# Optimization experiments

Measured on AMD Instinct MI355X. Metric: run time of the kernel, lower is better.

Reference implementation:

```python
import jax, jax.numpy as jnp
import numpy as np

PATCH_NUM = 10  # self.patch_num divisor
TOP_N = 5


def _extract_patches(feat, ps):
    """feat: [1,C,H,W] -> [P, C*ps*ps] with P = (H-ps)*(W-ps), matching the
    original loop over h in range(H-ps), w in range(W-ps)."""
    C, H, W = feat.shape[1:]
    Hm, Wm = H - ps, W - ps
    shifts = [feat[0, :, i:i + Hm, j:j + Wm] for i in range(ps) for j in range(ps)]
    patches = jnp.stack(shifts, axis=1)          # [C, ps*ps, Hm, Wm]
    return patches.reshape(C * ps * ps, Hm * Wm).T  # [P, K], P index = h*Wm + w


def _scale_loss(src_f, tgt_f, pos, ps):
    C = src_f.shape[1]
    K = C * ps * ps
    patches = _extract_patches(src_f, ps)  # [P, K]

    def per_target(p):
        th, tw = p[0], p[1]
        tpatch = jax.lax.dynamic_slice(tgt_f, (0, 0, th, tw), (1, C, ps, ps)).reshape(K)
        dist = jnp.sum(jnp.abs(patches - tpatch), axis=1)  # [P] summed L1 per patch
        _, ids = jax.lax.top_k(-dist, TOP_N)                # 5 nearest patches
        sel = patches[ids]                                   # [TOP_N, K]
        # sum over top-n of mean-L1, each divided by top_n (as in original)
        return jnp.sum(jnp.mean(jnp.abs(sel - tpatch), axis=1)) / TOP_N

    # sequential map over the small number of target patches keeps peak memory
    # at one [P,K] abs-diff buffer per step
    return jnp.sum(jax.lax.map(per_target, pos))


def setup_inputs() -> dict:
    key = jax.random.key(0)
    k0, k1, k2, k3, k4, k5 = jax.random.split(key, 6)
    return {
        "src_f0": jax.random.normal(k0, (1, 64, 256, 256), dtype=jnp.float32),
        "tgt_f0": jax.random.normal(k1, (1, 64, 256, 256), dtype=jnp.float32),
        "src_f1": jax.random.normal(k2, (1, 128, 128, 128), dtype=jnp.float32),
        "tgt_f1": jax.random.normal(k3, (1, 128, 128, 128), dtype=jnp.float32),
        "pos0": jax.random.randint(k4, (10, 2), 0, 253, dtype=jnp.int32),
        "pos1": jax.random.randint(k5, (5, 2), 0, 127, dtype=jnp.int32),
    }


def reference(src_f0, tgt_f0, src_f1, tgt_f1, pos0, pos1):
    loss = _scale_loss(src_f0, tgt_f0, pos0, 3) + _scale_loss(src_f1, tgt_f1, pos1, 1)
    return loss / PATCH_NUM
```

## Files before the change

kernel.cpp:

```cpp
#include <hip/hip_runtime.h>
#include <hip/hip_bf16.h>

#define BIG 3.4e38f


__device__ __forceinline__ void merge5(float a[5], const float* b) {
    float r[5];
#pragma unroll
    for (int k = 0; k < 5; ++k) {
        float best = BIG;
#pragma unroll
        for (int i = 0; i <= k + 1; ++i) {
            const int j = k + 1 - i;
            float va = (i == 0) ? -BIG : a[i - 1];
            float vb = (j == 0) ? -BIG : b[j - 1];
            best = fminf(best, fmaxf(va, vb));
        }
        r[k] = best;
    }
#pragma unroll
    for (int k = 0; k < 5; ++k) a[k] = r[k];
}

__device__ __forceinline__ void top5_insert(float m[5], float d) {
    if (d < m[4]) {
        m[4] = d;
#pragma unroll
        for (int k = 4; k > 0; --k) {
            float lo = fminf(m[k - 1], m[k]);
            float hi = fmaxf(m[k - 1], m[k]);
            m[k - 1] = lo;
            m[k] = hi;
        }
    }
}

__device__ __forceinline__ void wave_merge_top5(float m[5]) {
#pragma unroll
    for (int off = 1; off < 64; off <<= 1) {
        float o[5];
#pragma unroll
        for (int k = 0; k < 5; ++k) o[k] = __shfl_xor(m[k], off, 64);
        merge5(m, o);
    }
}

__device__ __forceinline__ bool block_merge_top5(float m[5], float (*s_top)[5],
                                                 float r[5]) {
    const int wid = threadIdx.x >> 6;
    if ((threadIdx.x & 63) == 0) {
#pragma unroll
        for (int k = 0; k < 5; ++k) s_top[wid][k] = m[k];
    }
    __syncthreads();
    if (threadIdx.x == 0) {
#pragma unroll
        for (int k = 0; k < 5; ++k) r[k] = s_top[0][k];
        merge5(r, s_top[1]);
        merge5(r, s_top[2]);
        merge5(r, s_top[3]);
        return true;
    }
    return false;
}

template <int CCH>
__global__ __launch_bounds__(256) void dist0_kernel(
    const float* __restrict__ src, const float* __restrict__ tgt,
    const int* __restrict__ pos, float* __restrict__ dist) {
    constexpr int H = 256, W = 256, HW = H * W, T = 10;
    constexpr int PLANE = 253 * 256;
    const int c0 = blockIdx.y * CCH;
    __shared__ float tl[T * CCH * 3 * 4];

    for (int idx = threadIdx.x; idx < T * CCH * 9; idx += 256) {
        int t = idx / (CCH * 9);
        int rem = idx - t * CCH * 9;
        int cc = rem / 9;
        int r2 = rem - cc * 9;
        int i = r2 / 3, j = r2 - i * 3;
        int th = pos[2 * t], tw = pos[2 * t + 1];
        tl[((t * CCH + cc) * 3 + i) * 4 + j] =
            tgt[(size_t)(c0 + cc) * HW + (th + i) * W + (tw + j)];
    }
    __syncthreads();

    const int tx = threadIdx.x & 63;
    const int ty = threadIdx.x >> 6;
    const int h = blockIdx.x * 4 + ty;
    const int hl = (h <= 250) ? h : 250;
    const int w0 = tx * 4;
    const int bw = (w0 <= 248) ? w0 + 4 : 248;

    float acc[T][4];
#pragma unroll
    for (int t = 0; t < T; ++t)
#pragma unroll
        for (int n = 0; n < 4; ++n) acc[t][n] = 0.f;

    const float* sb = src + (size_t)c0 * HW + hl * W;
    for (int cc = 0; cc < CCH; ++cc) {
        const float* row0 = sb + (size_t)cc * HW;
#pragma unroll
        for (int i = 0; i < 3; ++i) {
            const float4 a = *(const float4*)(row0 + i * W + w0);
            const float2 b = *(const float2*)(row0 + i * W + bw);
            const float r[6] = {a.x, a.y, a.z, a.w, b.x, b.y};
#pragma unroll
            for (int t = 0; t < T; ++t) {
                const float4 tv =
                    *(const float4*)&tl[((t * CCH + cc) * 3 + i) * 4];
#pragma unroll
                for (int n = 0; n < 4; ++n)
                    acc[t][n] += fabsf(r[n] - tv.x) + fabsf(r[n + 1] - tv.y) +
                                 fabsf(r[n + 2] - tv.z);
            }
        }
    }

    if (h < 253) {
        float* dp = dist + (size_t)blockIdx.y * T * PLANE + h * 256 + w0;
#pragma unroll
        for (int t = 0; t < T; ++t) {
            float4 o = {acc[t][0], acc[t][1], acc[t][2], acc[t][3]};
            *(float4*)(dp + (size_t)t * PLANE) = o;
        }
    }
}

template <int CCH>
__global__ __launch_bounds__(256) void dist1_kernel(
    const float* __restrict__ src, const float* __restrict__ tgt,
    const int* __restrict__ pos, float* __restrict__ dist) {
    constexpr int H = 128, W = 128, HW = H * W, T = 5;
    constexpr int PLANE = 127 * 128;
    const int c0 = blockIdx.y * CCH;
    __shared__ float tl[T * CCH];
    for (int idx = threadIdx.x; idx < T * CCH; idx += 256) {
        int t = idx / CCH, cc = idx - t * CCH;
        tl[idx] = tgt[(size_t)(c0 + cc) * HW + pos[2 * t] * W + pos[2 * t + 1]];
    }
    __syncthreads();

    const int w = threadIdx.x & 127;
    const int h = blockIdx.x * 2 + (threadIdx.x >> 7);
    float acc[T] = {0.f, 0.f, 0.f, 0.f, 0.f};
    const float* sp = src + (size_t)c0 * HW + h * W + w;
    for (int cc = 0; cc < CCH; ++cc) {
        const float v = sp[(size_t)cc * HW];
#pragma unroll
        for (int t = 0; t < T; ++t) acc[t] += fabsf(v - tl[t * CCH + cc]);
    }
    if (h < 127) {
        float* dp = dist + (size_t)blockIdx.y * T * PLANE + h * 128 + w;
#pragma unroll
        for (int t = 0; t < T; ++t) dp[(size_t)t * PLANE] = acc[t];
    }
}

template <int PLANE, int ROWW, int VALIDW, int NCH, int T, int NB>
__global__ __launch_bounds__(256) void top5_stage_kernel(
    const float* __restrict__ dist, float* __restrict__ part2) {
    __shared__ float s_top[4][5];
    const int t = blockIdx.y;
    constexpr int NF = PLANE / 4;
    constexpr int ITERS = (NF + NB * 256 - 1) / (NB * 256);
    float m[5] = {BIG, BIG, BIG, BIG, BIG};
#pragma unroll
    for (int k = 0; k < ITERS; ++k) {
        const int f = blockIdx.x * (ITERS * 256) + k * 256 + threadIdx.x;
        if (f < NF) {
            float4 s = *(const float4*)&dist[(size_t)t * PLANE + f * 4];
#pragma unroll
            for (int ch = 1; ch < NCH; ++ch) {
                float4 u =
                    *(const float4*)&dist[((size_t)ch * T + t) * PLANE + f * 4];
                s.x += u.x; s.y += u.y; s.z += u.z; s.w += u.w;
            }
            const int w0 = (f * 4) & (ROWW - 1);
            top5_insert(m, (w0 + 0 < VALIDW) ? s.x : BIG);
            top5_insert(m, (w0 + 1 < VALIDW) ? s.y : BIG);
            top5_insert(m, (w0 + 2 < VALIDW) ? s.z : BIG);
            top5_insert(m, (w0 + 3 < VALIDW) ? s.w : BIG);
        }
    }
    wave_merge_top5(m);
    float r[5];
    if (block_merge_top5(m, s_top, r)) {
        float* dst = part2 + (t * NB + blockIdx.x) * 5;
#pragma unroll
        for (int k = 0; k < 5; ++k) dst[k] = r[k];
    }
}

__global__ __launch_bounds__(256) void final_merge_kernel(
    const float* __restrict__ p2a, int na,
    const float* __restrict__ p2b, int nb,
    unsigned int* __restrict__ out) {
    __shared__ float s_sum[15];
    const int lane = threadIdx.x & 63;
    const int wv = threadIdx.x >> 6;
#pragma unroll
    for (int rt = 0; rt < 4; ++rt) {
        const int t = wv * 4 + rt;
        if (t < 15) {
            const float* base = (t < 10) ? p2a + t * na : p2b + (t - 10) * nb;
            const int n = (t < 10) ? na : nb;
            const float scale =
                (t < 10) ? 1.f / (576.f * 5.f) : 1.f / (128.f * 5.f);
            float m[5] = {BIG, BIG, BIG, BIG, BIG};
            for (int b0 = 0; b0 < n; b0 += 64)
                if (b0 + lane < n) top5_insert(m, base[b0 + lane]);
            wave_merge_top5(m);
            if (lane == 0)
                s_sum[t] = (m[0] + m[1] + m[2] + m[3] + m[4]) * scale;
        }
    }
    __syncthreads();
    if (threadIdx.x == 0) {
        float total = 0.f;
#pragma unroll
        for (int t = 0; t < 15; ++t) total += s_sum[t];
        union { float f; unsigned int i; } uf;
        uf.f = total * 0.1f;
        unsigned int bf = (uf.i + 0x7FFFu + ((uf.i >> 16) & 1u)) >> 16;
        out[0] = (uf.i & 0xFFFF0000u) | (bf & 0xFFFFu);
    }
}

template <int C, int H, int PS, int WM>
__global__ __launch_bounds__(256) void dist_top5_kernel(
    const float* __restrict__ src, const float* __restrict__ tgt,
    const int* __restrict__ pos, float* __restrict__ part) {
    constexpr int W = H;
    constexpr int K = C * PS * PS;
    constexpr int P = WM * WM;
    __shared__ float tlv[K];
    __shared__ float s_top[4][5];
    const int t = blockIdx.y;
    const int th = pos[2 * t], tw = pos[2 * t + 1];
    for (int idx = threadIdx.x; idx < K; idx += 256) {
        int c = idx / (PS * PS);
        int rem = idx - c * PS * PS;
        int i = rem / PS, j = rem - i * PS;
        tlv[idx] = tgt[(c * H + th + i) * W + tw + j];
    }
    __syncthreads();
    const int p = blockIdx.x * 256 + threadIdx.x;
    float d = BIG;
    if (p < P) {
        const int h = p / WM, w = p - h * WM;
        float acc = 0.f;
        for (int c = 0; c < C; ++c)
#pragma unroll
            for (int i = 0; i < PS; ++i) {
                const float* r = src + (c * H + h + i) * W + w;
                const float* tr = &tlv[(c * PS + i) * PS];
#pragma unroll
                for (int j = 0; j < PS; ++j) acc += fabsf(r[j] - tr[j]);
            }
        d = acc;
    }
    float m[5] = {d, BIG, BIG, BIG, BIG};
    wave_merge_top5(m);
    float r[5];
    if (block_merge_top5(m, s_top, r)) {
        float* dst = part + (t * gridDim.x + blockIdx.x) * 5;
#pragma unroll
        for (int k = 0; k < 5; ++k) dst[k] = r[k];
    }
}

extern "C" void kernel_launch(void* const* d_in, const int* in_sizes, int n_in,
                              void* d_out, int out_size, void* d_ws, size_t ws_size,
                              hipStream_t stream) {
    const float* src0 = (const float*)d_in[0];
    const float* tgt0 = (const float*)d_in[1];
    const float* src1 = (const float*)d_in[2];
    const float* tgt1 = (const float*)d_in[3];
    const int* pos0 = (const int*)d_in[4];
    const int* pos1 = (const int*)d_in[5];
    unsigned int* out = (unsigned int*)d_out;

    constexpr size_t PLANE0 = 253 * 256;
    constexpr size_t PLANE1 = 127 * 128;
    constexpr size_t P2 = 10 * 16 * 5 + 5 * 4 * 5;
    const size_t needA = (8 * 10 * PLANE0 + 8 * 5 * PLANE1 + P2) * 4;
    const size_t needB = (4 * 10 * PLANE0 + 4 * 5 * PLANE1 + P2) * 4;

    if (ws_size >= needA) {
        float* dist0 = (float*)d_ws;
        float* dist1 = dist0 + 8 * 10 * PLANE0;
        float* p2a = dist1 + 8 * 5 * PLANE1;
        float* p2b = p2a + 10 * 16 * 5;
        dist0_kernel<8><<<dim3(64, 8), 256, 0, stream>>>(src0, tgt0, pos0, dist0);
        dist1_kernel<16><<<dim3(64, 8), 256, 0, stream>>>(src1, tgt1, pos1, dist1);
        top5_stage_kernel<253 * 256, 256, 253, 8, 10, 16>
            <<<dim3(16, 10), 256, 0, stream>>>(dist0, p2a);
        top5_stage_kernel<127 * 128, 128, 127, 8, 5, 4>
            <<<dim3(4, 5), 256, 0, stream>>>(dist1, p2b);
        final_merge_kernel<<<dim3(1), 256, 0, stream>>>(p2a, 80, p2b, 20, out);
    } else if (ws_size >= needB) {
        float* dist0 = (float*)d_ws;
        float* dist1 = dist0 + 4 * 10 * PLANE0;
        float* p2a = dist1 + 4 * 5 * PLANE1;
        float* p2b = p2a + 10 * 16 * 5;
        dist0_kernel<16><<<dim3(64, 4), 256, 0, stream>>>(src0, tgt0, pos0, dist0);
        dist1_kernel<32><<<dim3(64, 4), 256, 0, stream>>>(src1, tgt1, pos1, dist1);
        top5_stage_kernel<253 * 256, 256, 253, 4, 10, 16>
            <<<dim3(16, 10), 256, 0, stream>>>(dist0, p2a);
        top5_stage_kernel<127 * 128, 128, 127, 4, 5, 4>
            <<<dim3(4, 5), 256, 0, stream>>>(dist1, p2b);
        final_merge_kernel<<<dim3(1), 256, 0, stream>>>(p2a, 80, p2b, 20, out);
    } else {
        float* part0 = (float*)d_ws;
        float* part1 = part0 + 10 * 251 * 5;
        dist_top5_kernel<64, 256, 3, 253>
            <<<dim3(251, 10), 256, 0, stream>>>(src0, tgt0, pos0, part0);
        dist_top5_kernel<128, 128, 1, 127>
            <<<dim3(64, 5), 256, 0, stream>>>(src1, tgt1, pos1, part1);
        final_merge_kernel<<<dim3(1), 256, 0, stream>>>(part0, 1255, part1, 320, out);
    }
}
```

Before: 139.8 us.

## Fuse scale-1 distance and top-5 into combined distance kernel

Merges the two distance kernels into one launch, with an extra grid row handling scale 1. That row processes all 128 channels and reduces top-5 per block in-kernel, so there is no scale-1 distance buffer and no separate top-5 stage. This removes two launches and a global write/read round trip. In exchange, the 64 scale-1 blocks each loop over 128 channels serially, which may become the tail of the fused kernel. The fallback workspace tier is also dropped.

```diff
diff --git a/kernel.cpp b/kernel.cpp
--- a/kernel.cpp
+++ b/kernel.cpp
@@ -64,97 +64,104 @@
     return false;
 }
 
-template <int CCH>
-__global__ __launch_bounds__(256) void dist0_kernel(
-    const float* __restrict__ src, const float* __restrict__ tgt,
-    const int* __restrict__ pos, float* __restrict__ dist) {
-    constexpr int H = 256, W = 256, HW = H * W, T = 10;
-    constexpr int PLANE = 253 * 256;
-    const int c0 = blockIdx.y * CCH;
-    __shared__ float tl[T * CCH * 3 * 4];
-
-    for (int idx = threadIdx.x; idx < T * CCH * 9; idx += 256) {
-        int t = idx / (CCH * 9);
-        int rem = idx - t * CCH * 9;
-        int cc = rem / 9;
-        int r2 = rem - cc * 9;
-        int i = r2 / 3, j = r2 - i * 3;
-        int th = pos[2 * t], tw = pos[2 * t + 1];
-        tl[((t * CCH + cc) * 3 + i) * 4 + j] =
-            tgt[(size_t)(c0 + cc) * HW + (th + i) * W + (tw + j)];
-    }
-    __syncthreads();
-
-    const int tx = threadIdx.x & 63;
-    const int ty = threadIdx.x >> 6;
-    const int h = blockIdx.x * 4 + ty;
-    const int hl = (h <= 250) ? h : 250;
-    const int w0 = tx * 4;
-    const int bw = (w0 <= 248) ? w0 + 4 : 248;
-
-    float acc[T][4];
-#pragma unroll
-    for (int t = 0; t < T; ++t)
-#pragma unroll
-        for (int n = 0; n < 4; ++n) acc[t][n] = 0.f;
-
-    const float* sb = src + (size_t)c0 * HW + hl * W;
-    for (int cc = 0; cc < CCH; ++cc) {
-        const float* row0 = sb + (size_t)cc * HW;
-#pragma unroll
-        for (int i = 0; i < 3; ++i) {
-            const float4 a = *(const float4*)(row0 + i * W + w0);
-            const float2 b = *(const float2*)(row0 + i * W + bw);
-            const float r[6] = {a.x, a.y, a.z, a.w, b.x, b.y};
+__global__ __launch_bounds__(256) void dist_all_kernel(
+    const float* __restrict__ src0, const float* __restrict__ tgt0,
+    const int* __restrict__ pos0, const float* __restrict__ src1,
+    const float* __restrict__ tgt1, const int* __restrict__ pos1,
+    float* __restrict__ dist0, float* __restrict__ p2b) {
+    __shared__ float tl[960];
+    __shared__ float s_top[4][5];
+
+    if (blockIdx.y < 8) {
+        constexpr int H = 256, W = 256, HW = H * W, T = 10, CCH = 8;
+        constexpr int PLANE = 253 * 256;
+        const int c0 = blockIdx.y * CCH;
+
+        for (int idx = threadIdx.x; idx < T * CCH * 9; idx += 256) {
+            int t = idx / (CCH * 9);
+            int rem = idx - t * (CCH * 9);
+            int cc = rem / 9;
+            int r2 = rem - cc * 9;
+            int i = r2 / 3, j = r2 - i * 3;
+            int th = pos0[2 * t], tw = pos0[2 * t + 1];
+            tl[((t * CCH + cc) * 3 + i) * 4 + j] =
+                tgt0[(size_t)(c0 + cc) * HW + (th + i) * W + (tw + j)];
+        }
+        __syncthreads();
+
+        const int tx = threadIdx.x & 63;
+        const int ty = threadIdx.x >> 6;
+        const int h = blockIdx.x * 4 + ty;
+        const int hl = (h <= 250) ? h : 250;
+        const int w0 = tx * 4;
+        const int bw = (w0 <= 248) ? w0 + 4 : 248;
+
+        float acc[T][4];
+#pragma unroll
+        for (int t = 0; t < T; ++t)
+#pragma unroll
+            for (int n = 0; n < 4; ++n) acc[t][n] = 0.f;
+
+        const float* sb = src0 + (size_t)c0 * HW + hl * W;
+        for (int cc = 0; cc < CCH; ++cc) {
+            const float* row0 = sb + (size_t)cc * HW;
+#pragma unroll
+            for (int i = 0; i < 3; ++i) {
+                const float4 a = *(const float4*)(row0 + i * W + w0);
+                const float2 b = *(const float2*)(row0 + i * W + bw);
+                const float r[6] = {a.x, a.y, a.z, a.w, b.x, b.y};
+#pragma unroll
+                for (int t = 0; t < T; ++t) {
+                    const float4 tv =
+                        *(const float4*)&tl[((t * CCH + cc) * 3 + i) * 4];
+#pragma unroll
+                    for (int n = 0; n < 4; ++n)
+                        acc[t][n] += fabsf(r[n] - tv.x) +
+                                     fabsf(r[n + 1] - tv.y) +
+                                     fabsf(r[n + 2] - tv.z);
+                }
+            }
+        }
+
+        if (h < 253) {
+            float* dp = dist0 + (size_t)blockIdx.y * T * PLANE + h * 256 + w0;
 #pragma unroll
             for (int t = 0; t < T; ++t) {
-                const float4 tv =
-                    *(const float4*)&tl[((t * CCH + cc) * 3 + i) * 4];
-#pragma unroll
-                for (int n = 0; n < 4; ++n)
-                    acc[t][n] += fabsf(r[n] - tv.x) + fabsf(r[n + 1] - tv.y) +
-                                 fabsf(r[n + 2] - tv.z);
-            }
-        }
-    }
-
-    if (h < 253) {
-        float* dp = dist + (size_t)blockIdx.y * T * PLANE + h * 256 + w0;
+                float4 o = {acc[t][0], acc[t][1], acc[t][2], acc[t][3]};
+                *(float4*)(dp + (size_t)t * PLANE) = o;
+            }
+        }
+    } else {
+        constexpr int H = 128, W = 128, HW = H * W, T = 5, C = 128;
+        for (int idx = threadIdx.x; idx < T * C; idx += 256) {
+            int t = idx / C, cc = idx - t * C;
+            tl[idx] =
+                tgt1[(size_t)cc * HW + pos1[2 * t] * W + pos1[2 * t + 1]];
+        }
+        __syncthreads();
+
+        const int w = threadIdx.x & 127;
+        const int h = blockIdx.x * 2 + (threadIdx.x >> 7);
+        float acc[T] = {0.f, 0.f, 0.f, 0.f, 0.f};
+        const float* sp = src1 + h * W + w;
+        for (int cc = 0; cc < C; ++cc) {
+            const float v = sp[(size_t)cc * HW];
+#pragma unroll
+            for (int t = 0; t < T; ++t) acc[t] += fabsf(v - tl[t * C + cc]);
+        }
+        const bool valid = (h < 127) && (w < 127);
 #pragma unroll
         for (int t = 0; t < T; ++t) {
-            float4 o = {acc[t][0], acc[t][1], acc[t][2], acc[t][3]};
-            *(float4*)(dp + (size_t)t * PLANE) = o;
-        }
-    }
-}
-
-template <int CCH>
-__global__ __launch_bounds__(256) void dist1_kernel(
-    const float* __restrict__ src, const float* __restrict__ tgt,
-    const int* __restrict__ pos, float* __restrict__ dist) {
-    constexpr int H = 128, W = 128, HW = H * W, T = 5;
-    constexpr int PLANE = 127 * 128;
-    const int c0 = blockIdx.y * CCH;
-    __shared__ float tl[T * CCH];
-    for (int idx = threadIdx.x; idx < T * CCH; idx += 256) {
-        int t = idx / CCH, cc = idx - t * CCH;
-        tl[idx] = tgt[(size_t)(c0 + cc) * HW + pos[2 * t] * W + pos[2 * t + 1]];
-    }
-    __syncthreads();
-
-    const int w = threadIdx.x & 127;
-    const int h = blockIdx.x * 2 + (threadIdx.x >> 7);
-    float acc[T] = {0.f, 0.f, 0.f, 0.f, 0.f};
-    const float* sp = src + (size_t)c0 * HW + h * W + w;
-    for (int cc = 0; cc < CCH; ++cc) {
-        const float v = sp[(size_t)cc * HW];
-#pragma unroll
-        for (int t = 0; t < T; ++t) acc[t] += fabsf(v - tl[t * CCH + cc]);
-    }
-    if (h < 127) {
-        float* dp = dist + (size_t)blockIdx.y * T * PLANE + h * 128 + w;
-#pragma unroll
-        for (int t = 0; t < T; ++t) dp[(size_t)t * PLANE] = acc[t];
+            float m[5] = {valid ? acc[t] : BIG, BIG, BIG, BIG, BIG};
+            wave_merge_top5(m);
+            float r[5];
+            if (block_merge_top5(m, s_top, r)) {
+                float* dst = p2b + (t * 64 + blockIdx.x) * 5;
+#pragma unroll
+                for (int k = 0; k < 5; ++k) dst[k] = r[k];
+            }
+            __syncthreads();
+        }
     }
 }
 
@@ -283,35 +290,20 @@
     unsigned int* out = (unsigned int*)d_out;
 
     constexpr size_t PLANE0 = 253 * 256;
-    constexpr size_t PLANE1 = 127 * 128;
-    constexpr size_t P2 = 10 * 16 * 5 + 5 * 4 * 5;
-    const size_t needA = (8 * 10 * PLANE0 + 8 * 5 * PLANE1 + P2) * 4;
-    const size_t needB = (4 * 10 * PLANE0 + 4 * 5 * PLANE1 + P2) * 4;
-
-    if (ws_size >= needA) {
+    constexpr size_t NP2A = 10 * 16 * 5;
+    constexpr size_t NP2B = 5 * 64 * 5;
+    const size_t need = (8 * 10 * PLANE0 + NP2A + NP2B) * 4;
+
+    if (ws_size >= need) {
         float* dist0 = (float*)d_ws;
-        float* dist1 = dist0 + 8 * 10 * PLANE0;
-        float* p2a = dist1 + 8 * 5 * PLANE1;
-        float* p2b = p2a + 10 * 16 * 5;
-        dist0_kernel<8><<<dim3(64, 8), 256, 0, stream>>>(src0, tgt0, pos0, dist0);
-        dist1_kernel<16><<<dim3(64, 8), 256, 0, stream>>>(src1, tgt1, pos1, dist1);
+        float* p2a = dist0 + 8 * 10 * PLANE0;
+        float* p2b = p2a + NP2A;
+
+        dist_all_kernel<<<dim3(64, 9), 256, 0, stream>>>(
+            src0, tgt0, pos0, src1, tgt1, pos1, dist0, p2b);
         top5_stage_kernel<253 * 256, 256, 253, 8, 10, 16>
             <<<dim3(16, 10), 256, 0, stream>>>(dist0, p2a);
-        top5_stage_kernel<127 * 128, 128, 127, 8, 5, 4>
-            <<<dim3(4, 5), 256, 0, stream>>>(dist1, p2b);
-        final_merge_kernel<<<dim3(1), 256, 0, stream>>>(p2a, 80, p2b, 20, out);
-    } else if (ws_size >= needB) {
-        float* dist0 = (float*)d_ws;
-        float* dist1 = dist0 + 4 * 10 * PLANE0;
-        float* p2a = dist1 + 4 * 5 * PLANE1;
-        float* p2b = p2a + 10 * 16 * 5;
-        dist0_kernel<16><<<dim3(64, 4), 256, 0, stream>>>(src0, tgt0, pos0, dist0);
-        dist1_kernel<32><<<dim3(64, 4), 256, 0, stream>>>(src1, tgt1, pos1, dist1);
-        top5_stage_kernel<253 * 256, 256, 253, 4, 10, 16>
-            <<<dim3(16, 10), 256, 0, stream>>>(dist0, p2a);
-        top5_stage_kernel<127 * 128, 128, 127, 4, 5, 4>
-            <<<dim3(4, 5), 256, 0, stream>>>(dist1, p2b);
-        final_merge_kernel<<<dim3(1), 256, 0, stream>>>(p2a, 80, p2b, 20, out);
+        final_merge_kernel<<<dim3(1), 256, 0, stream>>>(p2a, 80, p2b, 320, out);
     } else {
         float* part0 = (float*)d_ws;
         float* part1 = part0 + 10 * 251 * 5;
```

Result: faster. 132.3 us (-5.4%).
